# Kernel optimization log

Measured on AMD Instinct MI355X. Metric: run time of the kernel, lower is better.

## Reference

```python
import jax, jax.numpy as jnp
import numpy as np

D = 768
H = 12
HD = D // H
MLP = 3072
SCALE = 1.0 / np.sqrt(HD)
EPS = 1e-6


def setup_inputs() -> dict:
    key = jax.random.key(0)
    ks = jax.random.split(key, 16)
    s = 0.02
    inp = {
        "x": jax.random.normal(ks[0], (16, 1024, D), dtype=jnp.float32),
        "wq": jax.random.normal(ks[1], (D, D), dtype=jnp.float32) * s,
        "bq": jnp.zeros((D,), jnp.float32),
        "wk": jax.random.normal(ks[2], (D, D), dtype=jnp.float32) * s,
        "bk": jnp.zeros((D,), jnp.float32),
        "wv": jax.random.normal(ks[3], (D, D), dtype=jnp.float32) * s,
        "bv": jnp.zeros((D,), jnp.float32),
        "wo": jax.random.normal(ks[4], (D, D), dtype=jnp.float32) * s,
        "bo": jnp.zeros((D,), jnp.float32),
        "w1": jax.random.normal(ks[5], (D, MLP), dtype=jnp.float32) * s,
        "b1": jax.random.normal(ks[6], (MLP,), dtype=jnp.float32) * 1e-6,
        "w2": jax.random.normal(ks[7], (MLP, D), dtype=jnp.float32) * s,
        "b2": jax.random.normal(ks[8], (D,), dtype=jnp.float32) * 1e-6,
        "ln1_g": jnp.ones((D,), jnp.float32),
        "ln1_b": jnp.zeros((D,), jnp.float32),
        "ln2_g": jnp.ones((D,), jnp.float32),
        "ln2_b": jnp.zeros((D,), jnp.float32),
    }
    return inp


def layer_norm(x, g, b):
    mu = jnp.mean(x, axis=-1, keepdims=True)
    var = jnp.mean(jnp.square(x - mu), axis=-1, keepdims=True)
    return (x - mu) * jax.lax.rsqrt(var + EPS) * g + b


def block_fwd(x, wq, bq, wk, bk, wv, bv, wo, bo, w1, b1, w2, b2,
              ln1_g, ln1_b, ln2_g, ln2_b):
    B, N, _ = x.shape
    res = x
    h = layer_norm(x, ln1_g, ln1_b)
    # QKV projections, split into heads: [B, H, N, HD]
    q = (h @ wq + bq).reshape(B, N, H, HD).transpose(0, 2, 1, 3)
    k = (h @ wk + bk).reshape(B, N, H, HD).transpose(0, 2, 1, 3)
    v = (h @ wv + bv).reshape(B, N, H, HD).transpose(0, 2, 1, 3)
    scores = jnp.einsum("bhqd,bhkd->bhqk", q, k) * SCALE
    probs = jax.nn.softmax(scores, axis=-1)
    ctx = jnp.einsum("bhqk,bhkd->bhqd", probs, v)
    ctx = ctx.transpose(0, 2, 1, 3).reshape(B, N, D)
    attn_out = ctx @ wo + bo
    x = attn_out + res
    res = x
    h = layer_norm(x, ln2_g, ln2_b)
    h = jax.nn.gelu(h @ w1 + b1, approximate=False)
    h = h @ w2 + b2
    return h + res


def reference(x, wq, bq, wk, bk, wv, bv, wo, bo, w1, b1, w2, b2,
              ln1_g, ln1_b, ln2_g, ln2_b):
    return block_fwd(x, wq, bq, wk, bk, wv, bv, wo, bo, w1, b1, w2, b2,
                     ln1_g, ln1_b, ln2_g, ln2_b)
```

## Files before the change

### kernel.cpp

```cpp
#include <hip/hip_runtime.h>
#include <hip/hip_bf16.h>
#include <math.h>


#define BS   16
#define SEQ  1024
#define DIM  768
#define NH   12
#define HDM  64
#define MLPD 3072
#define NTOK (BS * SEQ)

typedef unsigned short u16;
typedef __attribute__((ext_vector_type(8))) short bf16x8;
typedef __attribute__((ext_vector_type(4))) float f32x4;

__device__ __forceinline__ float gelu_exact(float x) {
  return 0.5f * x * (1.0f + erff(x * 0.70710678118654752440f));
}
__device__ __forceinline__ u16 f2bf(float f) {
  __hip_bfloat16 h = __float2bfloat16(f);
  u16 r;
  __builtin_memcpy(&r, &h, 2);
  return r;
}
__device__ __forceinline__ u16 f2bf_sw(float f) {
  unsigned u = __float_as_uint(f);
  return (u16)((u + 0x7fffu + ((u >> 16) & 1u)) >> 16);
}

__global__ __launch_bounds__(256) void wtrans_kernel(
    const float* __restrict__ W, u16* __restrict__ Wt, int K, int N) {
  __shared__ u16 t[64][65];
  const int k0 = blockIdx.y << 6, n0 = blockIdx.x << 6;
  const int r  = threadIdx.x >> 2;
  const int c4 = (threadIdx.x & 3) << 4;
#pragma unroll
  for (int c = 0; c < 16; c += 4) {
    const float4 v = *(const float4*)(W + (size_t)(k0 + r) * N + n0 + c4 + c);
    t[r][c4 + c + 0] = f2bf_sw(v.x);
    t[r][c4 + c + 1] = f2bf_sw(v.y);
    t[r][c4 + c + 2] = f2bf_sw(v.z);
    t[r][c4 + c + 3] = f2bf_sw(v.w);
  }
  __syncthreads();
  unsigned wbuf[8];
#pragma unroll
  for (int p = 0; p < 8; ++p)
    wbuf[p] = (unsigned)t[c4 + 2 * p][r] | ((unsigned)t[c4 + 2 * p + 1][r] << 16);
  uint4* dst = (uint4*)(Wt + (size_t)(n0 + r) * K + k0 + c4);
  dst[0] = make_uint4(wbuf[0], wbuf[1], wbuf[2], wbuf[3]);
  dst[1] = make_uint4(wbuf[4], wbuf[5], wbuf[6], wbuf[7]);
}

__global__ __launch_bounds__(256) void ln_kernel(
    const float* __restrict__ x, const float* __restrict__ g,
    const float* __restrict__ b, u16* __restrict__ out) {
  const int lane = threadIdx.x & 63;
  const int wv   = threadIdx.x >> 6;
  const int tok  = (blockIdx.x << 2) + wv;
  const float4* xr = (const float4*)(x + (size_t)tok * DIM);
  float4 a0 = xr[lane], a1 = xr[lane + 64], a2 = xr[lane + 128];
  float s  = a0.x + a0.y + a0.z + a0.w + a1.x + a1.y + a1.z + a1.w
           + a2.x + a2.y + a2.z + a2.w;
  float s2 = a0.x*a0.x + a0.y*a0.y + a0.z*a0.z + a0.w*a0.w
           + a1.x*a1.x + a1.y*a1.y + a1.z*a1.z + a1.w*a1.w
           + a2.x*a2.x + a2.y*a2.y + a2.z*a2.z + a2.w*a2.w;
#pragma unroll
  for (int o = 32; o; o >>= 1) {
    s  += __shfl_xor(s,  o, 64);
    s2 += __shfl_xor(s2, o, 64);
  }
  const float mu   = s * (1.0f / DIM);
  const float rstd = rsqrtf(s2 * (1.0f / DIM) - mu * mu + 1e-6f);
  const float4* gp = (const float4*)g;
  const float4* bp = (const float4*)b;
  ushort4* op = (ushort4*)(out + (size_t)tok * DIM);
#define LN_EMIT(av, idx)                                                       \
  {                                                                            \
    const float4 gv = gp[idx]; const float4 bv = bp[idx]; ushort4 ov;          \
    ov.x = f2bf((av.x - mu) * rstd * gv.x + bv.x);                             \
    ov.y = f2bf((av.y - mu) * rstd * gv.y + bv.y);                             \
    ov.z = f2bf((av.z - mu) * rstd * gv.z + bv.z);                             \
    ov.w = f2bf((av.w - mu) * rstd * gv.w + bv.w);                             \
    op[idx] = ov;                                                              \
  }
  LN_EMIT(a0, lane);
  LN_EMIT(a1, lane + 64);
  LN_EMIT(a2, lane + 128);
#undef LN_EMIT
}

__device__ __forceinline__ void stage128x32(const u16* gtile, int ldk,
                                            u16* lds, int tid) {
#pragma unroll
  for (int i = 0; i < 2; ++i) {
    const int b = i * 4096 + tid * 16;
    const int row = b >> 6;
    const int chunk = (b >> 4) & 3;
    const u16* src = gtile + (size_t)row * ldk + chunk * 8;
    u16* dst = lds + ((i * 4096 + (tid >> 6) * 1024) >> 1);
    __builtin_amdgcn_global_load_lds((const void*)src, (void*)dst, 16, 0, 0);
  }
}

__device__ __forceinline__ void xcd_swizzle(int& bx, int& by) {
  const int nwg  = gridDim.x * gridDim.y;
  const int orig = blockIdx.y * gridDim.x + blockIdx.x;
  const int q8 = nwg >> 3, r8 = nwg & 7;
  const int xcd = orig & 7, sub = orig >> 3;
  const int wgid = (xcd < r8 ? xcd * (q8 + 1)
                             : r8 * (q8 + 1) + (xcd - r8) * q8) + sub;
  bx = wgid % gridDim.x;
  by = wgid / gridDim.x;
}

__device__ __forceinline__ void mm_core(const u16* Ab, const u16* Bb, int K,
                                        int tid, int wr, int wc, int fr,
                                        int kch, u16 (*As)[128 * 32],
                                        u16 (*Bs)[128 * 32], f32x4 acc[4][4]) {
  const int nkt = K >> 5;
  stage128x32(Ab, K, As[0], tid);
  stage128x32(Bb, K, Bs[0], tid);
  __syncthreads();
  int cur = 0;
  for (int kt = 0; kt < nkt; ++kt) {
    if (kt + 1 < nkt) {
      stage128x32(Ab + (kt + 1) * 32, K, As[cur ^ 1], tid);
      stage128x32(Bb + (kt + 1) * 32, K, Bs[cur ^ 1], tid);
    }
    bf16x8 af[4], bf[4];
#pragma unroll
    for (int f = 0; f < 4; ++f) {
      af[f] = *(const bf16x8*)&As[cur][(wr + (f << 4) + fr) * 32 + (kch << 3)];
      bf[f] = *(const bf16x8*)&Bs[cur][(wc + (f << 4) + fr) * 32 + (kch << 3)];
    }
#pragma unroll
    for (int i = 0; i < 4; ++i)
#pragma unroll
      for (int j = 0; j < 4; ++j)
        acc[i][j] = __builtin_amdgcn_mfma_f32_16x16x32_bf16(af[i], bf[j],
                                                            acc[i][j], 0, 0, 0);
    __syncthreads();
    cur ^= 1;
  }
}

template <int EPI>
__global__ __launch_bounds__(256) void mm_kernel(
    const u16* __restrict__ A, const u16* __restrict__ Wt,
    const float* __restrict__ bias, const float* res, void* outp,
    int M, int K, int Nc) {
  __shared__ __align__(16) u16 As[2][128 * 32];
  __shared__ __align__(16) u16 Bs[2][128 * 32];
  const int tid  = threadIdx.x;
  const int lane = tid & 63;
  const int wid  = tid >> 6;
  const int wr   = (wid >> 1) << 6;
  const int wc   = (wid & 1) << 6;
  int bx, by;
  xcd_swizzle(bx, by);
  const int row0 = by << 7;
  const int col0 = bx << 7;
  const int fr   = lane & 15;
  const int kch  = lane >> 4;

  f32x4 acc[4][4];
#pragma unroll
  for (int i = 0; i < 4; ++i)
#pragma unroll
    for (int j = 0; j < 4; ++j) acc[i][j] = {0.f, 0.f, 0.f, 0.f};

  mm_core(A + (size_t)row0 * K, Wt + (size_t)col0 * K, K, tid, wr, wc, fr,
          kch, As, Bs, acc);

  float* outf = (float*)outp;
  u16*   outb = (u16*)outp;
#pragma unroll
  for (int jf = 0; jf < 4; ++jf) {
    const int c = col0 + wc + (jf << 4) + fr;
    const float bv = bias[c];
#pragma unroll
    for (int i = 0; i < 4; ++i) {
#pragma unroll
      for (int j = 0; j < 4; ++j) {
        const int r = row0 + wr + (i << 4) + ((lane >> 4) << 2) + j;
        float v = acc[i][jf][j] + bv;
        if (EPI == 1) v += res[(size_t)r * Nc + c];
        if (EPI == 2) v = gelu_exact(v);
        if (EPI == 1) outf[(size_t)r * Nc + c] = v;
        else          outb[(size_t)r * Nc + c] = f2bf(v);
      }
    }
  }
}

__global__ __launch_bounds__(256) void mmqkv_kernel(
    const u16* __restrict__ A, const u16* __restrict__ Wt,
    const float* __restrict__ bq, const float* __restrict__ bk,
    const float* __restrict__ bv, u16* __restrict__ qb,
    u16* __restrict__ kb, u16* __restrict__ vtb) {
  __shared__ __align__(16) u16 As[2][128 * 32];
  __shared__ __align__(16) u16 Bs[2][128 * 32];
  const int tid  = threadIdx.x;
  const int lane = tid & 63;
  const int wid  = tid >> 6;
  const int wr   = (wid >> 1) << 6;
  const int wc   = (wid & 1) << 6;
  int bx, by;
  xcd_swizzle(bx, by);
  const int row0 = by << 7;
  const int col0 = bx << 7;
  const int fr   = lane & 15;
  const int kch  = lane >> 4;

  f32x4 acc[4][4];
#pragma unroll
  for (int i = 0; i < 4; ++i)
#pragma unroll
    for (int j = 0; j < 4; ++j) acc[i][j] = {0.f, 0.f, 0.f, 0.f};

  mm_core(A + (size_t)row0 * DIM, Wt + (size_t)col0 * DIM, DIM, tid, wr, wc,
          fr, kch, As, Bs, acc);

  const int sel = col0 >= 1536 ? 2 : (col0 >= 768 ? 1 : 0);
  const float* bias = sel == 0 ? bq : (sel == 1 ? bk : bv);
  const int cbase = col0 - sel * 768;
#pragma unroll
  for (int jf = 0; jf < 4; ++jf) {
    const int c = cbase + wc + (jf << 4) + fr;
    const float bvv = bias[c];
    if (sel == 2) {
      const int hh = c >> 6, dd = c & 63;
#pragma unroll
      for (int i = 0; i < 4; ++i) {
        const int rbase = row0 + wr + (i << 4) + ((lane >> 4) << 2);
        const int bb = rbase >> 10, n0 = rbase & 1023;
        ushort4 o;
        o.x = f2bf(acc[i][jf][0] + bvv);
        o.y = f2bf(acc[i][jf][1] + bvv);
        o.z = f2bf(acc[i][jf][2] + bvv);
        o.w = f2bf(acc[i][jf][3] + bvv);
        *(ushort4*)(vtb + ((((size_t)bb * NH + hh) * HDM + dd) << 10) + n0) = o;
      }
    } else {
      u16* dst = sel == 0 ? qb : kb;
      const float sc = sel == 0 ? 0.125f : 1.0f;
#pragma unroll
      for (int i = 0; i < 4; ++i)
#pragma unroll
        for (int j = 0; j < 4; ++j) {
          const int r = row0 + wr + (i << 4) + ((lane >> 4) << 2) + j;
          dst[(size_t)r * DIM + c] = f2bf((acc[i][jf][j] + bvv) * sc);
        }
    }
  }
}

__device__ __forceinline__ int swz(int row, int chunk) {
  return row * 128 + ((chunk ^ (row & 7)) << 4);
}

__global__ __launch_bounds__(256) void attn_kernel(
    const u16* __restrict__ q, const u16* __restrict__ k,
    const u16* __restrict__ vt, u16* __restrict__ ctx) {
  __shared__ __align__(16) u16 Qs[4096];
  __shared__ __align__(16) u16 Ks[2][4096];
  __shared__ __align__(16) u16 Vt[2][4096];
  __shared__ __align__(16) u16 Ps[4096];
  const int tid  = threadIdx.x;
  const int lane = tid & 63;
  const int w    = tid >> 6;
  const int fr   = lane & 15;
  const int g    = lane >> 4;
  const int qt = blockIdx.x, h = blockIdx.y, b = blockIdx.z;
  const size_t hbase = (size_t)b * SEQ * DIM + (size_t)h * HDM;
  const u16* vhd = vt + ((size_t)(b * NH + h) * HDM) * SEQ;
  const int srow = tid >> 2;
  const int sc   = (tid & 3) << 4;
  const int sch  = sc >> 3;

  {
    const u16* qp = q + hbase + (size_t)(qt * 64 + srow) * DIM + sc;
    const uint4 q0 = *(const uint4*)qp;
    const uint4 q1 = *(const uint4*)(qp + 8);
    *(uint4*)((char*)Qs + swz(srow, sch))     = q0;
    *(uint4*)((char*)Qs + swz(srow, sch + 1)) = q1;
  }
  {
    const u16* kp = k + hbase + (size_t)srow * DIM + sc;
    const u16* vp = vhd + (size_t)srow * SEQ + sc;
    const uint4 k0 = *(const uint4*)kp;
    const uint4 k1 = *(const uint4*)(kp + 8);
    const uint4 v0 = *(const uint4*)vp;
    const uint4 v1 = *(const uint4*)(vp + 8);
    *(uint4*)((char*)Ks[0] + swz(srow, sch))     = k0;
    *(uint4*)((char*)Ks[0] + swz(srow, sch + 1)) = k1;
    *(uint4*)((char*)Vt[0] + swz(srow, sch))     = v0;
    *(uint4*)((char*)Vt[0] + swz(srow, sch + 1)) = v1;
  }
  __syncthreads();

  float m_[4] = {-INFINITY, -INFINITY, -INFINITY, -INFINITY};
  float l_[4] = {0.f, 0.f, 0.f, 0.f};
  f32x4 oacc[4];
#pragma unroll
  for (int f = 0; f < 4; ++f) oacc[f] = {0.f, 0.f, 0.f, 0.f};

  int cur = 0;
  for (int kt = 0; kt < SEQ / 64; ++kt) {
    const bool pf = (kt + 1 < SEQ / 64);
    uint4 ka, kb2, va, vb2;
    if (pf) {
      const u16* kp = k + hbase + (size_t)((kt + 1) * 64 + srow) * DIM + sc;
      const u16* vp = vhd + (size_t)srow * SEQ + (kt + 1) * 64 + sc;
      ka  = *(const uint4*)kp;
      kb2 = *(const uint4*)(kp + 8);
      va  = *(const uint4*)vp;
      vb2 = *(const uint4*)(vp + 8);
    }
    const u16* ksc = Ks[cur];
    const u16* vtc = Vt[cur];

    f32x4 sacc[4];
#pragma unroll
    for (int f = 0; f < 4; ++f) sacc[f] = {0.f, 0.f, 0.f, 0.f};
    bf16x8 aq[2];
#pragma unroll
    for (int s = 0; s < 2; ++s)
      aq[s] = *(const bf16x8*)((char*)Qs + swz(w * 16 + fr, s * 4 + g));
#pragma unroll
    for (int f = 0; f < 4; ++f)
#pragma unroll
      for (int s = 0; s < 2; ++s) {
        const bf16x8 bk =
            *(const bf16x8*)((char*)ksc + swz(f * 16 + fr, s * 4 + g));
        sacc[f] = __builtin_amdgcn_mfma_f32_16x16x32_bf16(aq[s], bk, sacc[f],
                                                          0, 0, 0);
      }

    float corr[4];
#pragma unroll
    for (int r = 0; r < 4; ++r) {
      float rm = fmaxf(fmaxf(sacc[0][r], sacc[1][r]),
                       fmaxf(sacc[2][r], sacc[3][r]));
#pragma unroll
      for (int o = 8; o; o >>= 1) rm = fmaxf(rm, __shfl_xor(rm, o, 64));
      const float mnew = fmaxf(m_[r], rm);
      corr[r] = __expf(m_[r] - mnew);
      float ps = 0.f;
#pragma unroll
      for (int f = 0; f < 4; ++f) {
        const float p = __expf(sacc[f][r] - mnew);
        sacc[f][r] = p;
        ps += p;
      }
#pragma unroll
      for (int o = 8; o; o >>= 1) ps += __shfl_xor(ps, o, 64);
      l_[r] = l_[r] * corr[r] + ps;
      m_[r] = mnew;
#pragma unroll
      for (int f = 0; f < 4; ++f) oacc[f][r] *= corr[r];
    }

#pragma unroll
    for (int f = 0; f < 4; ++f)
#pragma unroll
      for (int r = 0; r < 4; ++r) {
        const int row = w * 16 + g * 4 + r;
        const int col = f * 16 + fr;
        *(u16*)((char*)Ps + ((row * 128 + col * 2) ^ ((row & 7) << 4))) =
            f2bf(sacc[f][r]);
      }

    bf16x8 ap[2];
#pragma unroll
    for (int s = 0; s < 2; ++s)
      ap[s] = *(const bf16x8*)((char*)Ps + swz(w * 16 + fr, s * 4 + g));
#pragma unroll
    for (int f = 0; f < 4; ++f)
#pragma unroll
      for (int s = 0; s < 2; ++s) {
        const bf16x8 bv =
            *(const bf16x8*)((char*)vtc + swz(f * 16 + fr, s * 4 + g));
        oacc[f] = __builtin_amdgcn_mfma_f32_16x16x32_bf16(ap[s], bv, oacc[f],
                                                          0, 0, 0);
      }

    if (pf) {
      u16* ksn = Ks[cur ^ 1];
      u16* vtn = Vt[cur ^ 1];
      *(uint4*)((char*)ksn + swz(srow, sch))     = ka;
      *(uint4*)((char*)ksn + swz(srow, sch + 1)) = kb2;
      *(uint4*)((char*)vtn + swz(srow, sch))     = va;
      *(uint4*)((char*)vtn + swz(srow, sch + 1)) = vb2;
      __syncthreads();
    }
    cur ^= 1;
  }

  float inv[4];
#pragma unroll
  for (int r = 0; r < 4; ++r) inv[r] = 1.0f / l_[r];
#pragma unroll
  for (int f = 0; f < 4; ++f)
#pragma unroll
    for (int r = 0; r < 4; ++r) {
      const int qrow = qt * 64 + w * 16 + g * 4 + r;
      ctx[hbase + (size_t)qrow * DIM + f * 16 + fr] = f2bf(oacc[f][r] * inv[r]);
    }
}

extern "C" void kernel_launch(void* const* d_in, const int* in_sizes, int n_in,
                              void* d_out, int out_size, void* d_ws,
                              size_t ws_size, hipStream_t stream) {
  const float* x    = (const float*)d_in[0];
  const float* wq   = (const float*)d_in[1];
  const float* bq   = (const float*)d_in[2];
  const float* wk   = (const float*)d_in[3];
  const float* bk   = (const float*)d_in[4];
  const float* wv   = (const float*)d_in[5];
  const float* bv   = (const float*)d_in[6];
  const float* wo   = (const float*)d_in[7];
  const float* bo   = (const float*)d_in[8];
  const float* w1   = (const float*)d_in[9];
  const float* b1   = (const float*)d_in[10];
  const float* w2   = (const float*)d_in[11];
  const float* b2   = (const float*)d_in[12];
  const float* ln1g = (const float*)d_in[13];
  const float* ln1b = (const float*)d_in[14];
  const float* ln2g = (const float*)d_in[15];
  const float* ln2b = (const float*)d_in[16];
  float* out = (float*)d_out;

  const size_t TD = (size_t)NTOK * DIM;
  const size_t S768 = (size_t)DIM * DIM;
  const size_t SMLP = (size_t)DIM * MLPD;
  u16* wtq  = (u16*)d_ws;
  u16* wtk  = wtq + S768;
  u16* wtv  = wtk + S768;
  u16* wto  = wtv + S768;
  u16* wt1  = wto + S768;
  u16* wt2  = wt1 + SMLP;
  u16* tokb = wt2 + SMLP;
  u16* big  = tokb + TD;
  u16* qb   = big;
  u16* kb   = big + TD;
  u16* vtb  = big + 2 * TD;

  const dim3 blk(256);
  wtrans_kernel<<<dim3(DIM / 64, DIM / 64), blk, 0, stream>>>(wq, wtq, DIM, DIM);
  wtrans_kernel<<<dim3(DIM / 64, DIM / 64), blk, 0, stream>>>(wk, wtk, DIM, DIM);
  wtrans_kernel<<<dim3(DIM / 64, DIM / 64), blk, 0, stream>>>(wv, wtv, DIM, DIM);
  wtrans_kernel<<<dim3(DIM / 64, DIM / 64), blk, 0, stream>>>(wo, wto, DIM, DIM);
  wtrans_kernel<<<dim3(MLPD / 64, DIM / 64), blk, 0, stream>>>(w1, wt1, DIM, MLPD);
  wtrans_kernel<<<dim3(DIM / 64, MLPD / 64), blk, 0, stream>>>(w2, wt2, MLPD, DIM);
  ln_kernel<<<dim3(NTOK / 4), blk, 0, stream>>>(x, ln1g, ln1b, tokb);
  mmqkv_kernel<<<dim3(18, NTOK / 128), blk, 0, stream>>>(
      tokb, wtq, bq, bk, bv, qb, kb, vtb);
  attn_kernel<<<dim3(SEQ / 64, NH, BS), blk, 0, stream>>>(qb, kb, vtb, tokb);
  const dim3 g768(DIM / 128, NTOK / 128);
  mm_kernel<1><<<g768, blk, 0, stream>>>(tokb, wto, bo, x, out, NTOK, DIM, DIM);
  ln_kernel<<<dim3(NTOK / 4), blk, 0, stream>>>(out, ln2g, ln2b, tokb);
  mm_kernel<2><<<dim3(MLPD / 128, NTOK / 128), blk, 0, stream>>>(
      tokb, wt1, b1, nullptr, big, NTOK, DIM, MLPD);
  mm_kernel<1><<<g768, blk, 0, stream>>>(big, wt2, b2, out, out, NTOK, MLPD, DIM);
}
```

Baseline: 772.5 us.

## Single-buffer attention K/V tiles, add MFMA priority hints and lazy softmax rescale

The attention kernel moves from double-buffered K/V shared tiles to single buffers, which cuts LDS use from 40KB to 24KB so more blocks can fit per CU. In exchange it needs an extra barrier before each tile overwrite. It also raises wave priority around the MFMA sequences with s_setprio. It adds a lazy online-softmax path that skips the max update and accumulator rescale when every row's new max stays within 8 of the running max. That path lowers exp and multiply work but relies on the bounded-growth check to keep values safe.

```diff
diff --git a/kernel.cpp b/kernel.cpp
--- a/kernel.cpp
+++ b/kernel.cpp
@@ -265,8 +265,8 @@
     const u16* __restrict__ q, const u16* __restrict__ k,
     const u16* __restrict__ vt, u16* __restrict__ ctx) {
   __shared__ __align__(16) u16 Qs[4096];
-  __shared__ __align__(16) u16 Ks[2][4096];
-  __shared__ __align__(16) u16 Vt[2][4096];
+  __shared__ __align__(16) u16 Ks[4096];
+  __shared__ __align__(16) u16 Vt[4096];
   __shared__ __align__(16) u16 Ps[4096];
   const int tid  = threadIdx.x;
   const int lane = tid & 63;
@@ -286,18 +286,16 @@
     const uint4 q1 = *(const uint4*)(qp + 8);
     *(uint4*)((char*)Qs + swz(srow, sch))     = q0;
     *(uint4*)((char*)Qs + swz(srow, sch + 1)) = q1;
-  }
-  {
     const u16* kp = k + hbase + (size_t)srow * DIM + sc;
     const u16* vp = vhd + (size_t)srow * SEQ + sc;
     const uint4 k0 = *(const uint4*)kp;
     const uint4 k1 = *(const uint4*)(kp + 8);
     const uint4 v0 = *(const uint4*)vp;
     const uint4 v1 = *(const uint4*)(vp + 8);
-    *(uint4*)((char*)Ks[0] + swz(srow, sch))     = k0;
-    *(uint4*)((char*)Ks[0] + swz(srow, sch + 1)) = k1;
-    *(uint4*)((char*)Vt[0] + swz(srow, sch))     = v0;
-    *(uint4*)((char*)Vt[0] + swz(srow, sch + 1)) = v1;
+    *(uint4*)((char*)Ks + swz(srow, sch))     = k0;
+    *(uint4*)((char*)Ks + swz(srow, sch + 1)) = k1;
+    *(uint4*)((char*)Vt + swz(srow, sch))     = v0;
+    *(uint4*)((char*)Vt + swz(srow, sch + 1)) = v1;
   }
   __syncthreads();
 
@@ -307,7 +305,6 @@
 #pragma unroll
   for (int f = 0; f < 4; ++f) oacc[f] = {0.f, 0.f, 0.f, 0.f};
 
-  int cur = 0;
   for (int kt = 0; kt < SEQ / 64; ++kt) {
     const bool pf = (kt + 1 < SEQ / 64);
     uint4 ka, kb2, va, vb2;
@@ -319,8 +316,6 @@
       va  = *(const uint4*)vp;
       vb2 = *(const uint4*)(vp + 8);
     }
-    const u16* ksc = Ks[cur];
-    const u16* vtc = Vt[cur];
 
     f32x4 sacc[4];
 #pragma unroll
@@ -329,38 +324,62 @@
 #pragma unroll
     for (int s = 0; s < 2; ++s)
       aq[s] = *(const bf16x8*)((char*)Qs + swz(w * 16 + fr, s * 4 + g));
+    __builtin_amdgcn_s_setprio(1);
 #pragma unroll
     for (int f = 0; f < 4; ++f)
 #pragma unroll
       for (int s = 0; s < 2; ++s) {
         const bf16x8 bk =
-            *(const bf16x8*)((char*)ksc + swz(f * 16 + fr, s * 4 + g));
+            *(const bf16x8*)((char*)Ks + swz(f * 16 + fr, s * 4 + g));
         sacc[f] = __builtin_amdgcn_mfma_f32_16x16x32_bf16(aq[s], bk, sacc[f],
                                                           0, 0, 0);
       }
-
-    float corr[4];
+    __builtin_amdgcn_s_setprio(0);
+
+    float rm[4];
 #pragma unroll
     for (int r = 0; r < 4; ++r) {
-      float rm = fmaxf(fmaxf(sacc[0][r], sacc[1][r]),
-                       fmaxf(sacc[2][r], sacc[3][r]));
-#pragma unroll
-      for (int o = 8; o; o >>= 1) rm = fmaxf(rm, __shfl_xor(rm, o, 64));
-      const float mnew = fmaxf(m_[r], rm);
-      corr[r] = __expf(m_[r] - mnew);
-      float ps = 0.f;
-#pragma unroll
-      for (int f = 0; f < 4; ++f) {
-        const float p = __expf(sacc[f][r] - mnew);
-        sacc[f][r] = p;
-        ps += p;
-      }
-#pragma unroll
-      for (int o = 8; o; o >>= 1) ps += __shfl_xor(ps, o, 64);
-      l_[r] = l_[r] * corr[r] + ps;
-      m_[r] = mnew;
-#pragma unroll
-      for (int f = 0; f < 4; ++f) oacc[f][r] *= corr[r];
+      float t = fmaxf(fmaxf(sacc[0][r], sacc[1][r]),
+                      fmaxf(sacc[2][r], sacc[3][r]));
+#pragma unroll
+      for (int o = 8; o; o >>= 1) t = fmaxf(t, __shfl_xor(t, o, 64));
+      rm[r] = t;
+    }
+    const bool ok = (rm[0] <= m_[0] + 8.f) && (rm[1] <= m_[1] + 8.f) &&
+                    (rm[2] <= m_[2] + 8.f) && (rm[3] <= m_[3] + 8.f);
+    if (__all(ok)) {
+#pragma unroll
+      for (int r = 0; r < 4; ++r) {
+        float ps = 0.f;
+#pragma unroll
+        for (int f = 0; f < 4; ++f) {
+          const float p = __expf(sacc[f][r] - m_[r]);
+          sacc[f][r] = p;
+          ps += p;
+        }
+#pragma unroll
+        for (int o = 8; o; o >>= 1) ps += __shfl_xor(ps, o, 64);
+        l_[r] += ps;
+      }
+    } else {
+#pragma unroll
+      for (int r = 0; r < 4; ++r) {
+        const float mnew = fmaxf(m_[r], rm[r]);
+        const float corr = __expf(m_[r] - mnew);
+        float ps = 0.f;
+#pragma unroll
+        for (int f = 0; f < 4; ++f) {
+          const float p = __expf(sacc[f][r] - mnew);
+          sacc[f][r] = p;
+          ps += p;
+        }
+#pragma unroll
+        for (int o = 8; o; o >>= 1) ps += __shfl_xor(ps, o, 64);
+        l_[r] = l_[r] * corr + ps;
+        m_[r] = mnew;
+#pragma unroll
+        for (int f = 0; f < 4; ++f) oacc[f][r] *= corr;
+      }
     }
 
 #pragma unroll
@@ -377,26 +396,26 @@
 #pragma unroll
     for (int s = 0; s < 2; ++s)
       ap[s] = *(const bf16x8*)((char*)Ps + swz(w * 16 + fr, s * 4 + g));
+    __builtin_amdgcn_s_setprio(1);
 #pragma unroll
     for (int f = 0; f < 4; ++f)
 #pragma unroll
       for (int s = 0; s < 2; ++s) {
         const bf16x8 bv =
-            *(const bf16x8*)((char*)vtc + swz(f * 16 + fr, s * 4 + g));
+            *(const bf16x8*)((char*)Vt + swz(f * 16 + fr, s * 4 + g));
         oacc[f] = __builtin_amdgcn_mfma_f32_16x16x32_bf16(ap[s], bv, oacc[f],
                                                           0, 0, 0);
       }
-
+    __builtin_amdgcn_s_setprio(0);
+
+    __syncthreads();
     if (pf) {
-      u16* ksn = Ks[cur ^ 1];
-      u16* vtn = Vt[cur ^ 1];
-      *(uint4*)((char*)ksn + swz(srow, sch))     = ka;
-      *(uint4*)((char*)ksn + swz(srow, sch + 1)) = kb2;
-      *(uint4*)((char*)vtn + swz(srow, sch))     = va;
-      *(uint4*)((char*)vtn + swz(srow, sch + 1)) = vb2;
+      *(uint4*)((char*)Ks + swz(srow, sch))     = ka;
+      *(uint4*)((char*)Ks + swz(srow, sch + 1)) = kb2;
+      *(uint4*)((char*)Vt + swz(srow, sch))     = va;
+      *(uint4*)((char*)Vt + swz(srow, sch + 1)) = vb2;
       __syncthreads();
     }
-    cur ^= 1;
   }
 
   float inv[4];
```

After: 771.9 us. No clear change (-0.1%).
